# Performance work log

Measured on AMD Instinct MI355X. Metric: run time of the kernel, lower is better.

The kernel has to match this reference:

```python
import jax, jax.numpy as jnp
import numpy as np

B, NX, NH, NY, K = 4096, 512, 512, 256, 8


def setup_inputs() -> dict:
    key = jax.random.key(0)
    k0, k1, k2, k3, k4, k5 = jax.random.split(key, 6)
    s = 1.0 / np.sqrt(NH)  # torch RNNCell init scale
    x = jax.random.normal(k0, (B, NX), jnp.float32)
    h = jax.random.normal(k1, (B, NH), jnp.float32)
    pi = jax.random.uniform(k2, (B, K), jnp.float32)
    pi = pi / pi.sum(axis=1, keepdims=True)  # __init_belief normalizes to sum 1
    W_ih = jax.random.uniform(k3, (K, NH, NX), jnp.float32, minval=-s, maxval=s)
    W_hh = jax.random.uniform(k4, (K, NH, NH), jnp.float32, minval=-s, maxval=s)
    W_out = jax.random.uniform(k5, (NY, NH), jnp.float32, minval=-s, maxval=s)
    return {"x": x, "h": h, "pi": pi, "W_ih": W_ih, "W_hh": W_hh, "W_out": W_out}


def reference(x, h, pi, W_ih, W_hh, W_out):
    # Per-state RNN cells (bias=False): h_k[:, :, k] = tanh(x @ W_ih[k].T + h @ W_hh[k].T)
    h_k = jnp.tanh(
        jnp.einsum('bx,knx->bnk', x, W_ih)
        + jnp.einsum('bh,knh->bnk', h, W_hh)
    )  # (B, NH, K)
    # out_k = out_layer applied per state: (B, NY, K)
    out_k = jnp.einsum('bnk,yn->byk', h_k, W_out)
    # belief-weighted soft combination of hidden states: states[b] = h_k[b] @ pi[b]
    h_mix = jnp.einsum('bnk,bk->bn', h_k, pi)  # (B, NH)
    out = h_mix @ W_out.T  # (B, NY)
    return (out, h_mix, out_k, h_k)
```

## Files before the change

### kernel.cpp

```cpp
#include <hip/hip_runtime.h>
#include <hip/hip_bf16.h>
#include <stdint.h>

typedef unsigned short u16;
typedef __attribute__((ext_vector_type(8))) short short8;
typedef __attribute__((ext_vector_type(4))) float f32x4;

#define BATCH 4096
#define OFF_OUT  0
#define OFF_HMIX (BATCH * 256)
#define OFF_OK   (OFF_HMIX + BATCH * 512)
#define OFF_HK   (OFF_OK + BATCH * 256 * 8)

#define WS_XB   0
#define WS_HB   (2097152)
#define WS_WIH  (4194304)
#define WS_WHH  (6291456)
#define WS_WOUT (8388608)

__device__ __forceinline__ u16 f2b(float f) {
  union { float f; uint32_t u; } c; c.f = f;
  uint32_t u = c.u;
  return (u16)((u + 0x7fffu + ((u >> 16) & 1u)) >> 16);
}

__device__ __forceinline__ void gload16(const u16* g, u16* l) {
  __builtin_amdgcn_global_load_lds(
      (const __attribute__((address_space(1))) void*)g,
      (__attribute__((address_space(3))) void*)l, 16, 0, 0);
}

__global__ __launch_bounds__(256) void k0_cvt(
    const float* __restrict__ x, const float* __restrict__ h,
    const float* __restrict__ Wih, const float* __restrict__ Whh,
    const float* __restrict__ Wout, u16* __restrict__ ws) {
  const int i = blockIdx.x * 256 + threadIdx.x;
  const float* src; int j; size_t dst;
  if      (i <  524288) { src = x;    j = i;           dst = WS_XB;   }
  else if (i < 1048576) { src = h;    j = i -  524288; dst = WS_HB;   }
  else if (i < 1572864) { src = Wih;  j = i - 1048576; dst = WS_WIH;  }
  else if (i < 2097152) { src = Whh;  j = i - 1572864; dst = WS_WHH;  }
  else                  { src = Wout; j = i - 2097152; dst = WS_WOUT; }
  const float4 v = ((const float4*)src)[j];
  ushort4 o;
  o.x = f2b(v.x); o.y = f2b(v.y); o.z = f2b(v.z); o.w = f2b(v.w);
  ((ushort4*)(ws + dst))[j] = o;
}

__global__ __launch_bounds__(256) void k1_gemm_tanh(
    const u16* __restrict__ xb, const u16* __restrict__ hb,
    const u16* __restrict__ Wih, const u16* __restrict__ Whh,
    float* __restrict__ T) {
  __shared__ u16 As[128 * 64];
  __shared__ u16 Bs[128 * 64];
  const int tid  = threadIdx.x;
  const int lane = tid & 63;
  const int w    = tid >> 6;
  const int wm   = w >> 1, wn = w & 1;
  const int row0 = blockIdx.x * 128;
  const int col0 = blockIdx.y * 128;
  const int kk   = col0 >> 9;
  const int nh0  = col0 & 511;
  const int sr   = tid >> 3;
  const int sc   = (tid & 7) * 8;
  const int ldsw = (w * 8) * 64;

  const u16* WihK = Wih + (size_t)kk * 512 * 512;
  const u16* WhhK = Whh + (size_t)kk * 512 * 512;

  f32x4 acc[4][4] = {};

  for (int kt = 0; kt < 16; ++kt) {
    const int kb = kt * 64;
    const u16* Asrc; const u16* Bsrc; int ko;
    if (kb < 512) { Asrc = xb; Bsrc = WihK; ko = kb; }
    else          { Asrc = hb; Bsrc = WhhK; ko = kb - 512; }
#pragma unroll
    for (int ro = 0; ro < 4; ++ro) {
      gload16(Asrc + (size_t)(row0 + ro * 32 + sr) * 512 + ko + sc, &As[ro * 32 * 64 + ldsw]);
      gload16(Bsrc + (size_t)(nh0  + ro * 32 + sr) * 512 + ko + sc, &Bs[ro * 32 * 64 + ldsw]);
    }
    __syncthreads();
#pragma unroll
    for (int ks = 0; ks < 2; ++ks) {
      const int koff = ks * 32 + (lane >> 4) * 8;
      short8 af[4], bf[4];
#pragma unroll
      for (int i = 0; i < 4; ++i)
        af[i] = *(const short8*)&As[(wm * 64 + i * 16 + (lane & 15)) * 64 + koff];
#pragma unroll
      for (int j = 0; j < 4; ++j)
        bf[j] = *(const short8*)&Bs[(wn * 64 + j * 16 + (lane & 15)) * 64 + koff];
#pragma unroll
      for (int i = 0; i < 4; ++i)
#pragma unroll
        for (int j = 0; j < 4; ++j)
          acc[i][j] = __builtin_amdgcn_mfma_f32_16x16x32_bf16(af[i], bf[j], acc[i][j], 0, 0, 0);
    }
    __syncthreads();
  }

  const int quad = lane >> 4, cl = lane & 15;
#pragma unroll
  for (int i = 0; i < 4; ++i)
#pragma unroll
    for (int j = 0; j < 4; ++j)
#pragma unroll
      for (int r = 0; r < 4; ++r) {
        const int rr = row0 + wm * 64 + i * 16 + quad * 4 + r;
        const int cc = col0 + wn * 64 + j * 16 + cl;
        const float v = acc[i][j][r];
        const float e = __expf(2.0f * v);
        T[(size_t)rr * 4096 + cc] = 1.0f - 2.0f / (e + 1.0f);
      }
}

__global__ __launch_bounds__(256) void k2_gemm_out(
    const float* __restrict__ T, const u16* __restrict__ Wout,
    float* __restrict__ O) {
  __shared__ u16 As[128 * 64];
  __shared__ u16 Bs[128 * 64];
  const int tid  = threadIdx.x;
  const int lane = tid & 63;
  const int w    = tid >> 6;
  const int wm   = w >> 1, wn = w & 1;
  const int row0 = blockIdx.x * 128;
  const int y0   = blockIdx.y * 128;
  const int kk   = blockIdx.z;
  const int sr   = tid >> 3;
  const int sc   = (tid & 7) * 8;
  const int ldsw = (w * 8) * 64;

  f32x4 acc[4][4] = {};

  for (int kt = 0; kt < 8; ++kt) {
    const int kb = kt * 64;
#pragma unroll
    for (int ro = 0; ro < 4; ++ro) {
      const float* src = T + (size_t)(row0 + ro * 32 + sr) * 4096 + kk * 512 + kb + sc;
      const float4 v0 = *(const float4*)(src);
      const float4 v1 = *(const float4*)(src + 4);
      short8 cv;
      cv[0] = (short)f2b(v0.x); cv[1] = (short)f2b(v0.y);
      cv[2] = (short)f2b(v0.z); cv[3] = (short)f2b(v0.w);
      cv[4] = (short)f2b(v1.x); cv[5] = (short)f2b(v1.y);
      cv[6] = (short)f2b(v1.z); cv[7] = (short)f2b(v1.w);
      *(short8*)&As[(ro * 32 + sr) * 64 + sc] = cv;
      gload16(Wout + (size_t)(y0 + ro * 32 + sr) * 512 + kb + sc,
              &Bs[ro * 32 * 64 + ldsw]);
    }
    __syncthreads();
#pragma unroll
    for (int ks = 0; ks < 2; ++ks) {
      const int koff = ks * 32 + (lane >> 4) * 8;
      short8 af[4], bf[4];
#pragma unroll
      for (int i = 0; i < 4; ++i)
        af[i] = *(const short8*)&As[(wm * 64 + i * 16 + (lane & 15)) * 64 + koff];
#pragma unroll
      for (int j = 0; j < 4; ++j)
        bf[j] = *(const short8*)&Bs[(wn * 64 + j * 16 + (lane & 15)) * 64 + koff];
#pragma unroll
      for (int i = 0; i < 4; ++i)
#pragma unroll
        for (int j = 0; j < 4; ++j)
          acc[i][j] = __builtin_amdgcn_mfma_f32_16x16x32_bf16(af[i], bf[j], acc[i][j], 0, 0, 0);
    }
    __syncthreads();
  }

  const int quad = lane >> 4, cl = lane & 15;
#pragma unroll
  for (int i = 0; i < 4; ++i)
#pragma unroll
    for (int j = 0; j < 4; ++j)
#pragma unroll
      for (int r = 0; r < 4; ++r) {
        const int rr = row0 + wm * 64 + i * 16 + quad * 4 + r;
        const int cc = y0 + wn * 64 + j * 16 + cl;
        O[(size_t)rr * 2048 + kk * 256 + cc] = acc[i][j][r];
      }
}

__global__ __launch_bounds__(512) void k3_epi(const float* __restrict__ pi,
                                              float* __restrict__ dout) {
  const int b   = blockIdx.x;
  const int tid = threadIdx.x;
  float* T = dout + OFF_HK;
  float* O = dout + OFF_OK;

  float pif[8];
#pragma unroll
  for (int k = 0; k < 8; ++k) pif[k] = pi[b * 8 + k];

  float tv[8]; float hm = 0.0f;
#pragma unroll
  for (int k = 0; k < 8; ++k) {
    const float v = T[(size_t)b * 4096 + k * 512 + tid];
    tv[k] = v; hm += pif[k] * v;
  }
  float ov[8]; float om = 0.0f;
  if (tid < 256) {
#pragma unroll
    for (int k = 0; k < 8; ++k) {
      const float v = O[(size_t)b * 2048 + k * 256 + tid];
      ov[k] = v; om += pif[k] * v;
    }
  }
  __syncthreads();

  float4* tw = (float4*)&T[(size_t)b * 4096 + tid * 8];
  tw[0] = make_float4(tv[0], tv[1], tv[2], tv[3]);
  tw[1] = make_float4(tv[4], tv[5], tv[6], tv[7]);
  dout[OFF_HMIX + (size_t)b * 512 + tid] = hm;

  if (tid < 256) {
    float4* ow = (float4*)&O[(size_t)b * 2048 + tid * 8];
    ow[0] = make_float4(ov[0], ov[1], ov[2], ov[3]);
    ow[1] = make_float4(ov[4], ov[5], ov[6], ov[7]);
    dout[OFF_OUT + (size_t)b * 256 + tid] = om;
  }
}

extern "C" void kernel_launch(void* const* d_in, const int* in_sizes, int n_in,
                              void* d_out, int out_size, void* d_ws, size_t ws_size,
                              hipStream_t stream) {
  const float* x    = (const float*)d_in[0];
  const float* h    = (const float*)d_in[1];
  const float* pi   = (const float*)d_in[2];
  const float* Wih  = (const float*)d_in[3];
  const float* Whh  = (const float*)d_in[4];
  const float* Wout = (const float*)d_in[5];
  float* out = (float*)d_out;
  u16* ws  = (u16*)d_ws;
  float* T = out + OFF_HK;
  float* O = out + OFF_OK;

  k0_cvt<<<dim3(8320), 256, 0, stream>>>(x, h, Wih, Whh, Wout, ws);
  k1_gemm_tanh<<<dim3(32, 32), 256, 0, stream>>>(
      ws + WS_XB, ws + WS_HB, ws + WS_WIH, ws + WS_WHH, T);
  k2_gemm_out<<<dim3(32, 2, 8), 256, 0, stream>>>(T, ws + WS_WOUT, O);
  k3_epi<<<dim3(BATCH), 512, 0, stream>>>(pi, out);
}
```

Measured before the change: 243.1 us.

## Store tanh intermediate as bf16 in workspace and XOR-swizzle LDS tiles

The tanh GEMM now writes its intermediate as bf16 into workspace instead of fp32 into the output. The output GEMM can then load it with direct global-to-LDS copies instead of loading fp32 and converting in registers, and the epilogue reads bf16 and writes fp32 h_k. Both GEMMs also XOR-swizzle the 16-byte column chunk in LDS by row to reduce bank conflicts on fragment reads. This halves intermediate traffic, but h_k output now carries bf16 rounding, which costs precision.

```diff
diff --git a/kernel.cpp b/kernel.cpp
--- a/kernel.cpp
+++ b/kernel.cpp
@@ -17,7 +17,11 @@
 #define WS_WIH  (4194304)
 #define WS_WHH  (6291456)
 #define WS_WOUT (8388608)
-
+#define WS_T    (8519680)
+
+__device__ __forceinline__ float b2f(u16 v) {
+  union { uint32_t u; float f; } c; c.u = ((uint32_t)v) << 16; return c.f;
+}
 __device__ __forceinline__ u16 f2b(float f) {
   union { float f; uint32_t u; } c; c.f = f;
   uint32_t u = c.u;
@@ -50,7 +54,7 @@
 __global__ __launch_bounds__(256) void k1_gemm_tanh(
     const u16* __restrict__ xb, const u16* __restrict__ hb,
     const u16* __restrict__ Wih, const u16* __restrict__ Whh,
-    float* __restrict__ T) {
+    u16* __restrict__ Tb) {
   __shared__ u16 As[128 * 64];
   __shared__ u16 Bs[128 * 64];
   const int tid  = threadIdx.x;
@@ -62,7 +66,7 @@
   const int kk   = col0 >> 9;
   const int nh0  = col0 & 511;
   const int sr   = tid >> 3;
-  const int sc   = (tid & 7) * 8;
+  const int sc   = ((tid & 7) ^ ((tid >> 3) & 7)) * 8;
   const int ldsw = (w * 8) * 64;
 
   const u16* WihK = Wih + (size_t)kk * 512 * 512;
@@ -81,16 +85,17 @@
       gload16(Bsrc + (size_t)(nh0  + ro * 32 + sr) * 512 + ko + sc, &Bs[ro * 32 * 64 + ldsw]);
     }
     __syncthreads();
+    const int l7 = lane & 7, quad = lane >> 4, rl = lane & 15;
 #pragma unroll
     for (int ks = 0; ks < 2; ++ks) {
-      const int koff = ks * 32 + (lane >> 4) * 8;
       short8 af[4], bf[4];
-#pragma unroll
-      for (int i = 0; i < 4; ++i)
-        af[i] = *(const short8*)&As[(wm * 64 + i * 16 + (lane & 15)) * 64 + koff];
+      const int cs = ((ks * 4 + quad) ^ l7) * 8;
+#pragma unroll
+      for (int i = 0; i < 4; ++i)
+        af[i] = *(const short8*)&As[(wm * 64 + i * 16 + rl) * 64 + cs];
 #pragma unroll
       for (int j = 0; j < 4; ++j)
-        bf[j] = *(const short8*)&Bs[(wn * 64 + j * 16 + (lane & 15)) * 64 + koff];
+        bf[j] = *(const short8*)&Bs[(wn * 64 + j * 16 + rl) * 64 + cs];
 #pragma unroll
       for (int i = 0; i < 4; ++i)
 #pragma unroll
@@ -111,12 +116,12 @@
         const int cc = col0 + wn * 64 + j * 16 + cl;
         const float v = acc[i][j][r];
         const float e = __expf(2.0f * v);
-        T[(size_t)rr * 4096 + cc] = 1.0f - 2.0f / (e + 1.0f);
+        Tb[(size_t)rr * 4096 + cc] = f2b(1.0f - 2.0f / (e + 1.0f));
       }
 }
 
 __global__ __launch_bounds__(256) void k2_gemm_out(
-    const float* __restrict__ T, const u16* __restrict__ Wout,
+    const u16* __restrict__ Tb, const u16* __restrict__ Wout,
     float* __restrict__ O) {
   __shared__ u16 As[128 * 64];
   __shared__ u16 Bs[128 * 64];
@@ -128,7 +133,7 @@
   const int y0   = blockIdx.y * 128;
   const int kk   = blockIdx.z;
   const int sr   = tid >> 3;
-  const int sc   = (tid & 7) * 8;
+  const int sc   = ((tid & 7) ^ ((tid >> 3) & 7)) * 8;
   const int ldsw = (w * 8) * 64;
 
   f32x4 acc[4][4] = {};
@@ -137,29 +142,23 @@
     const int kb = kt * 64;
 #pragma unroll
     for (int ro = 0; ro < 4; ++ro) {
-      const float* src = T + (size_t)(row0 + ro * 32 + sr) * 4096 + kk * 512 + kb + sc;
-      const float4 v0 = *(const float4*)(src);
-      const float4 v1 = *(const float4*)(src + 4);
-      short8 cv;
-      cv[0] = (short)f2b(v0.x); cv[1] = (short)f2b(v0.y);
-      cv[2] = (short)f2b(v0.z); cv[3] = (short)f2b(v0.w);
-      cv[4] = (short)f2b(v1.x); cv[5] = (short)f2b(v1.y);
-      cv[6] = (short)f2b(v1.z); cv[7] = (short)f2b(v1.w);
-      *(short8*)&As[(ro * 32 + sr) * 64 + sc] = cv;
+      gload16(Tb + (size_t)(row0 + ro * 32 + sr) * 4096 + kk * 512 + kb + sc,
+              &As[ro * 32 * 64 + ldsw]);
       gload16(Wout + (size_t)(y0 + ro * 32 + sr) * 512 + kb + sc,
               &Bs[ro * 32 * 64 + ldsw]);
     }
     __syncthreads();
+    const int l7 = lane & 7, quad = lane >> 4, rl = lane & 15;
 #pragma unroll
     for (int ks = 0; ks < 2; ++ks) {
-      const int koff = ks * 32 + (lane >> 4) * 8;
       short8 af[4], bf[4];
-#pragma unroll
-      for (int i = 0; i < 4; ++i)
-        af[i] = *(const short8*)&As[(wm * 64 + i * 16 + (lane & 15)) * 64 + koff];
+      const int cs = ((ks * 4 + quad) ^ l7) * 8;
+#pragma unroll
+      for (int i = 0; i < 4; ++i)
+        af[i] = *(const short8*)&As[(wm * 64 + i * 16 + rl) * 64 + cs];
 #pragma unroll
       for (int j = 0; j < 4; ++j)
-        bf[j] = *(const short8*)&Bs[(wn * 64 + j * 16 + (lane & 15)) * 64 + koff];
+        bf[j] = *(const short8*)&Bs[(wn * 64 + j * 16 + rl) * 64 + cs];
 #pragma unroll
       for (int i = 0; i < 4; ++i)
 #pragma unroll
@@ -183,10 +182,10 @@
 }
 
 __global__ __launch_bounds__(512) void k3_epi(const float* __restrict__ pi,
+                                              const u16* __restrict__ Tb,
                                               float* __restrict__ dout) {
   const int b   = blockIdx.x;
   const int tid = threadIdx.x;
-  float* T = dout + OFF_HK;
   float* O = dout + OFF_OK;
 
   float pif[8];
@@ -196,7 +195,7 @@
   float tv[8]; float hm = 0.0f;
 #pragma unroll
   for (int k = 0; k < 8; ++k) {
-    const float v = T[(size_t)b * 4096 + k * 512 + tid];
+    const float v = b2f(Tb[(size_t)b * 4096 + k * 512 + tid]);
     tv[k] = v; hm += pif[k] * v;
   }
   float ov[8]; float om = 0.0f;
@@ -209,7 +208,7 @@
   }
   __syncthreads();
 
-  float4* tw = (float4*)&T[(size_t)b * 4096 + tid * 8];
+  float4* tw = (float4*)&dout[OFF_HK + (size_t)b * 4096 + tid * 8];
   tw[0] = make_float4(tv[0], tv[1], tv[2], tv[3]);
   tw[1] = make_float4(tv[4], tv[5], tv[6], tv[7]);
   dout[OFF_HMIX + (size_t)b * 512 + tid] = hm;
@@ -233,12 +232,11 @@
   const float* Wout = (const float*)d_in[5];
   float* out = (float*)d_out;
   u16* ws  = (u16*)d_ws;
-  float* T = out + OFF_HK;
   float* O = out + OFF_OK;
 
   k0_cvt<<<dim3(8320), 256, 0, stream>>>(x, h, Wih, Whh, Wout, ws);
   k1_gemm_tanh<<<dim3(32, 32), 256, 0, stream>>>(
-      ws + WS_XB, ws + WS_HB, ws + WS_WIH, ws + WS_WHH, T);
-  k2_gemm_out<<<dim3(32, 2, 8), 256, 0, stream>>>(T, ws + WS_WOUT, O);
-  k3_epi<<<dim3(BATCH), 512, 0, stream>>>(pi, out);
-}
+      ws + WS_XB, ws + WS_HB, ws + WS_WIH, ws + WS_WHH, ws + WS_T);
+  k2_gemm_out<<<dim3(32, 2, 8), 256, 0, stream>>>(ws + WS_T, ws + WS_WOUT, O);
+  k3_epi<<<dim3(BATCH), 512, 0, stream>>>(pi, ws + WS_T, out);
+}
```

Measured after the change: 226.7 us. -6.7%, faster.
